# Optimization experiments

Hardware: AMD Instinct MI355X
Metric: run time of the kernel (lower is better)

## Reference

```python
import jax, jax.numpy as jnp
import numpy as np

V, D, H, L, F, S_MAX = 30522, 768, 12, 12, 3072, 512
B, S = 4, 512
HD = D // H
EPS = 1e-5

def setup_inputs():
    key = jax.random.key(0)
    ks = jax.random.split(key, 16)
    s = 0.02
    inp = {
        'input_ids': jax.random.randint(ks[0], (B, S), 0, V),
        'attention_mask': jnp.ones((B, S), dtype=jnp.int32),
        'word_emb': jax.random.normal(ks[1], (V, D)) * s,
        'pos_emb': jax.random.normal(ks[2], (S_MAX, D)) * s,
        'seg_emb': jax.random.normal(ks[3], (2, D)) * s,
        'emb_ln_g': jnp.ones((D,)), 'emb_ln_b': jnp.zeros((D,)),
        # per-layer stacked params, leading dim L
        'Wq': jax.random.normal(ks[4], (L, D, D)) * s,
        'Wk': jax.random.normal(ks[5], (L, D, D)) * s,
        'Wv': jax.random.normal(ks[6], (L, D, D)) * s,
        'Wo': jax.random.normal(ks[7], (L, D, D)) * s,
        'ff1_w': jax.random.normal(ks[8], (L, D, F)) * s,
        'ff1_b': jnp.zeros((L, F)),
        'ff2_w': jax.random.normal(ks[9], (L, F, D)) * s,
        'ff2_b': jnp.zeros((L, D)),
        'ln1_g': jnp.ones((L, D)), 'ln1_b': jnp.zeros((L, D)),
        'ln2_g': jnp.ones((L, D)), 'ln2_b': jnp.zeros((L, D)),
        'out_w': jax.random.normal(ks[10], (D, V)) * s,
        'out_b': jnp.zeros((V,)),
    }
    return inp

def _ln(x, g, b):
    mu = jnp.mean(x, axis=-1, keepdims=True)
    var = jnp.mean(jnp.square(x - mu), axis=-1, keepdims=True)
    return (x - mu) * jax.lax.rsqrt(var + EPS) * g + b

def reference(input_ids, attention_mask, word_emb, pos_emb, seg_emb,
              emb_ln_g, emb_ln_b, Wq, Wk, Wv, Wo, ff1_w, ff1_b, ff2_w, ff2_b,
              ln1_g, ln1_b, ln2_g, ln2_b, out_w, out_b):
    b, s = input_ids.shape
    # embeddings: word + position + segment (segment ids are all zero buffer)
    emb = word_emb[input_ids] + pos_emb[:s][None, :, :] + seg_emb[0][None, None, :]
    x = _ln(emb, emb_ln_g, emb_ln_b)  # [B,S,D]
    # key-position mask: True where masked out. [B,1,1,S]
    neg_mask = (attention_mask == 0)[:, None, None, :]
    scale = 1.0 / jnp.sqrt(jnp.asarray(D, x.dtype))  # NOTE: embed_dim, not head_dim

    def layer(x, p):
        wq, wk, wv, wo, f1w, f1b, f2w, f2b, g1, b1, g2, b2 = p
        q = (x @ wq).reshape(b, s, H, HD)
        k = (x @ wk).reshape(b, s, H, HD)
        v = (x @ wv).reshape(b, s, H, HD)
        scores = jnp.einsum('bqhd,bkhd->bhqk', q, k) * scale  # [B,H,S,S]
        scores = jnp.where(neg_mask, -jnp.inf, scores)
        attn = jax.nn.softmax(scores, axis=-1)
        o = jnp.einsum('bhqk,bkhd->bqhd', attn, v).reshape(b, s, D) @ wo
        x1 = _ln(x + o, g1, b1)
        h = jax.nn.gelu(x1 @ f1w + f1b, approximate=False)  # torch GELU is exact erf
        x2 = _ln(x1 + h @ f2w + f2b, g2, b2)
        return x2, attn

    x, attn_scores = jax.lax.scan(
        layer, x,
        (Wq, Wk, Wv, Wo, ff1_w, ff1_b, ff2_w, ff2_b, ln1_g, ln1_b, ln2_g, ln2_b))
    logits = x @ out_w + out_b  # [B,S,V]
    return logits, attn_scores  # attn_scores: [L,B,H,S,S]
```

## Files before the change

kernel.cpp:

```cpp
#include <hip/hip_runtime.h>
#include <hip/hip_bf16.h>

#define NLAYER 12
#define DMODEL 768
#define NHEAD  12
#define HDIM   64
#define FDIM   3072
#define VOCAB  30522
#define SLEN   512
#define NBATCH 4
#define NTOK   (NBATCH*SLEN)
#define EPSLN  1e-5f

typedef unsigned short u16;
using bf16 = __hip_bfloat16;
typedef __bf16 bf16x8 __attribute__((ext_vector_type(8)));
typedef float  f32x4  __attribute__((ext_vector_type(4)));
typedef u16    u16x4  __attribute__((ext_vector_type(4)));

__device__ __forceinline__ u16 f2bs(float f) {
    bf16 h = __float2bfloat16(f);
    return *reinterpret_cast<u16*>(&h);
}

__device__ __forceinline__ void gload_lds16(const void* g, void* l) {
    auto gp = (const __attribute__((address_space(1))) unsigned int*)g;
    auto lp = (__attribute__((address_space(3))) unsigned int*)(unsigned long long)l;
    __builtin_amdgcn_global_load_lds(gp, lp, 16, 0, 0);
}

template<int N> __device__ __forceinline__ void waitv() {
    if constexpr (N == 0)      asm volatile("s_waitcnt vmcnt(0)" ::: "memory");
    else if constexpr (N == 3) asm volatile("s_waitcnt vmcnt(3)" ::: "memory");
    else if constexpr (N == 4) asm volatile("s_waitcnt vmcnt(4)" ::: "memory");
    else if constexpr (N == 6) asm volatile("s_waitcnt vmcnt(6)" ::: "memory");
    else if constexpr (N == 8) asm volatile("s_waitcnt vmcnt(8)" ::: "memory");
}

__device__ __forceinline__ float wave_sum64(float v) {
#pragma unroll
    for (int off = 32; off > 0; off >>= 1) v += __shfl_down(v, off, 64);
    return v;
}
__device__ __forceinline__ float block_sum256(float v, float* red) {
    v = wave_sum64(v);
    __syncthreads();
    if ((threadIdx.x & 63) == 0) red[threadIdx.x >> 6] = v;
    __syncthreads();
    return red[0] + red[1] + red[2] + red[3];
}

__global__ __launch_bounds__(256) void embed_ln_kernel(
    const int* __restrict__ ids, const float* __restrict__ word,
    const float* __restrict__ pos, const float* __restrict__ seg,
    const float* __restrict__ g, const float* __restrict__ b,
    float* __restrict__ out, u16* __restrict__ outb)
{
    __shared__ float red[4];
    int t = blockIdx.x;
    int s = t & (SLEN - 1);
    long woff = (long)ids[t] * DMODEL;
    float vals[3];
#pragma unroll
    for (int i = 0; i < 3; i++) {
        int d = threadIdx.x + i * 256;
        vals[i] = word[woff + d] + pos[(long)s * DMODEL + d] + seg[d];
    }
    float mu = block_sum256(vals[0] + vals[1] + vals[2], red) * (1.0f / DMODEL);
    float vv = 0.f;
#pragma unroll
    for (int i = 0; i < 3; i++) { float d0 = vals[i] - mu; vv += d0 * d0; }
    float rstd = rsqrtf(block_sum256(vv, red) * (1.0f / DMODEL) + EPSLN);
#pragma unroll
    for (int i = 0; i < 3; i++) {
        int d = threadIdx.x + i * 256;
        float r = (vals[i] - mu) * rstd * g[d] + b[d];
        out[(long)t * DMODEL + d] = r;
        outb[(long)t * DMODEL + d] = f2bs(r);
    }
}

__global__ __launch_bounds__(256) void ln_res2_kernel(
    const float* __restrict__ a, const float* __restrict__ p0,
    const float* __restrict__ p1, const float* __restrict__ cbias,
    const float* __restrict__ g, const float* __restrict__ beta,
    float* __restrict__ out, u16* __restrict__ outb)
{
    __shared__ float red[4];
    long t = blockIdx.x;
    float vals[3];
#pragma unroll
    for (int i = 0; i < 3; i++) {
        int d = threadIdx.x + i * 256;
        float bb = cbias ? cbias[d] : 0.f;
        vals[i] = a[t * DMODEL + d] + p0[t * DMODEL + d] + p1[t * DMODEL + d] + bb;
    }
    float mu = block_sum256(vals[0] + vals[1] + vals[2], red) * (1.0f / DMODEL);
    float vv = 0.f;
#pragma unroll
    for (int i = 0; i < 3; i++) { float d0 = vals[i] - mu; vv += d0 * d0; }
    float rstd = rsqrtf(block_sum256(vv, red) * (1.0f / DMODEL) + EPSLN);
#pragma unroll
    for (int i = 0; i < 3; i++) {
        int d = threadIdx.x + i * 256;
        float r = (vals[i] - mu) * rstd * g[d] + beta[d];
        out[t * DMODEL + d] = r;
        outb[t * DMODEL + d] = f2bs(r);
    }
}

#define DD (DMODEL*DMODEL)
#define DF (DMODEL*FDIM)
#define LAYER_W_ELEMS (4*DD + 2*DF)
#define TILES_DD 576
#define TILES_DF 2304
#define TILES_LAYER (4*TILES_DD + 2*TILES_DF)
#define TILES_ALL (NLAYER*TILES_LAYER)
#define NTX_OW ((VOCAB + 31) / 32)
#define TILES_OW (NTX_OW * (DMODEL/32))

__global__ __launch_bounds__(256) void conv_all_kernel(
    const float* __restrict__ Wq, const float* __restrict__ Wk,
    const float* __restrict__ Wv, const float* __restrict__ Wo,
    const float* __restrict__ F1w, const float* __restrict__ F2w,
    const float* __restrict__ OutW, u16* __restrict__ wT, u16* __restrict__ owT)
{
    __shared__ float t[32][33];
    int id = blockIdx.x;
    const float* src; u16* dst; int K, N, tt;
    if (id < TILES_ALL) {
        int l = id / TILES_LAYER, r = id - l * TILES_LAYER;
        u16* base = wT + (long)l * LAYER_W_ELEMS;
        if (r < TILES_DD)           { src = Wq  + (long)l * DD; dst = base;            K = DMODEL; N = DMODEL; tt = r; }
        else if (r < 2 * TILES_DD)  { src = Wk  + (long)l * DD; dst = base + DD;       K = DMODEL; N = DMODEL; tt = r - TILES_DD; }
        else if (r < 3 * TILES_DD)  { src = Wv  + (long)l * DD; dst = base + 2 * DD;   K = DMODEL; N = DMODEL; tt = r - 2 * TILES_DD; }
        else if (r < 4 * TILES_DD)  { src = Wo  + (long)l * DD; dst = base + 3 * DD;   K = DMODEL; N = DMODEL; tt = r - 3 * TILES_DD; }
        else if (r < 4 * TILES_DD + TILES_DF)
                                    { src = F1w + (long)l * DF; dst = base + 4 * DD;   K = DMODEL; N = FDIM;   tt = r - 4 * TILES_DD; }
        else                        { src = F2w + (long)l * DF; dst = base + 4 * DD + DF; K = FDIM; N = DMODEL; tt = r - 4 * TILES_DD - TILES_DF; }
    } else {
        src = OutW; dst = owT; K = DMODEL; N = VOCAB; tt = id - TILES_ALL;
    }
    int ntx = (N + 31) >> 5;
    int n0 = (tt % ntx) * 32, k0 = (tt / ntx) * 32;
    int tx = threadIdx.x & 31, ty = threadIdx.x >> 5;
#pragma unroll
    for (int i = 0; i < 32; i += 8) {
        int k = k0 + ty + i, n = n0 + tx;
        t[ty + i][tx] = (k < K && n < N) ? src[(long)k * N + n] : 0.f;
    }
    __syncthreads();
#pragma unroll
    for (int i = 0; i < 32; i += 8) {
        int n = n0 + ty + i, k = k0 + tx;
        if (n < N && k < K) dst[(long)n * K + k] = f2bs(t[tx][ty + i]);
    }
}

__global__ __launch_bounds__(256, 2) void attn_kernel(
    const u16* __restrict__ qkvb, const u16* __restrict__ vtb,
    const int* __restrict__ amask,
    float* __restrict__ attn, u16* __restrict__ ob)
{
    __shared__ u16 Qs[64][64];
    __shared__ u16 Ks[SLEN][64];
    __shared__ float maskadd[SLEN];
    __shared__ __align__(16) float redA[64][4];
    __shared__ __align__(16) float redB[64][4];

    u16* Ph = &Ks[0][0];
    u16* Vh = &Ks[256][0];

    int z = blockIdx.y;
    int b = z / NHEAD, h = z - b * NHEAD;
    int m0 = blockIdx.x * 64;
    int tid = threadIdx.x;
    int wave = tid >> 6, lane = tid & 63;
    int quad = lane >> 4, l16 = lane & 15;
    const float scale2 = 0.036084391824351615f * 1.4426950408889634f;

    for (int i = tid; i < SLEN; i += 256)
        maskadd[i] = amask[b * SLEN + i] ? 0.f : -1e30f;

    const u16* Qbase = qkvb + (long)(b * SLEN) * (3 * DMODEL) + h * HDIM;
    const u16* Kbase = Qbase + DMODEL;
    const u16* Vtbase = vtb + (long)z * HDIM * SLEN;

#pragma unroll
    for (int i = 0; i < 2; i++) {
        int off = wave * 2048 + i * 1024 + lane * 16;
        int row = off >> 7, c = (off >> 4) & 7, g = c ^ (row & 7);
        gload_lds16(Qbase + (long)(m0 + row) * (3 * DMODEL) + g * 8,
                    (char*)&Qs[0][0] + wave * 2048 + i * 1024);
    }
#pragma unroll
    for (int i = 0; i < 16; i++) {
        int off = wave * 16384 + i * 1024 + lane * 16;
        int row = off >> 7, c = (off >> 4) & 7, g = c ^ (row & 7);
        gload_lds16(Kbase + (long)row * (3 * DMODEL) + g * 8,
                    (char*)&Ks[0][0] + wave * 16384 + i * 1024);
    }
    __syncthreads();

    f32x4 acc[4][8];
#pragma unroll
    for (int i = 0; i < 4; i++)
#pragma unroll
        for (int j = 0; j < 8; j++) acc[i][j] = (f32x4){0.f, 0.f, 0.f, 0.f};

#pragma unroll
    for (int ks = 0; ks < 2; ks++) {
        bf16x8 afr[4], bfr[8];
#pragma unroll
        for (int i = 0; i < 4; i++) {
            int row = i * 16 + l16;
            int slot = ((ks << 2) + quad) ^ (row & 7);
            afr[i] = *reinterpret_cast<const bf16x8*>((char*)&Qs[0][0] + row * 128 + slot * 16);
        }
#pragma unroll
        for (int j = 0; j < 8; j++) {
            int row = wave * 128 + j * 16 + l16;
            int slot = ((ks << 2) + quad) ^ (row & 7);
            bfr[j] = *reinterpret_cast<const bf16x8*>((char*)&Ks[0][0] + row * 128 + slot * 16);
        }
#pragma unroll
        for (int i = 0; i < 4; i++)
#pragma unroll
            for (int j = 0; j < 8; j++)
                acc[i][j] = __builtin_amdgcn_mfma_f32_16x16x32_bf16(afr[i], bfr[j], acc[i][j], 0, 0, 0);
    }

    {
        float ma[8];
#pragma unroll
        for (int j = 0; j < 8; j++) ma[j] = maskadd[wave * 128 + j * 16 + l16];
#pragma unroll
        for (int i = 0; i < 4; i++)
#pragma unroll
            for (int j = 0; j < 8; j++)
#pragma unroll
                for (int r = 0; r < 4; r++)
                    acc[i][j][r] = acc[i][j][r] * scale2 + ma[j];
    }

    float rmax[4][4];
#pragma unroll
    for (int i = 0; i < 4; i++)
#pragma unroll
        for (int r = 0; r < 4; r++) {
            float m = -3e38f;
#pragma unroll
            for (int j = 0; j < 8; j++) m = fmaxf(m, acc[i][j][r]);
            rmax[i][r] = m;
        }
#pragma unroll
    for (int off = 1; off < 16; off <<= 1)
#pragma unroll
        for (int i = 0; i < 4; i++)
#pragma unroll
            for (int r = 0; r < 4; r++)
                rmax[i][r] = fmaxf(rmax[i][r], __shfl_xor(rmax[i][r], off, 64));
    if (l16 == 0) {
#pragma unroll
        for (int i = 0; i < 4; i++)
#pragma unroll
            for (int r = 0; r < 4; r++) redA[i * 16 + quad * 4 + r][wave] = rmax[i][r];
    }
    __syncthreads();

    {
        const u16* Vb = Vtbase + 0;
#pragma unroll
        for (int i = 0; i < 8; i++) {
            int o = wave * 8192 + i * 1024 + lane * 16;
            int hd = o >> 9, c = (o >> 4) & 31, g = c ^ (hd & 7);
            gload_lds16(Vb + (long)hd * SLEN + g * 8, (char*)Vh + wave * 8192 + i * 1024);
        }
    }

#pragma unroll
    for (int i = 0; i < 4; i++)
#pragma unroll
        for (int r = 0; r < 4; r++) {
            f32x4 v = *reinterpret_cast<const f32x4*>(&redA[i * 16 + quad * 4 + r][0]);
            rmax[i][r] = fmaxf(fmaxf(v[0], v[1]), fmaxf(v[2], v[3]));
        }

    float rsum[4][4];
#pragma unroll
    for (int i = 0; i < 4; i++)
#pragma unroll
        for (int r = 0; r < 4; r++) {
            float s = 0.f;
#pragma unroll
            for (int j = 0; j < 8; j++) {
                float e = __builtin_amdgcn_exp2f(acc[i][j][r] - rmax[i][r]);
                acc[i][j][r] = e;
                s += e;
            }
            rsum[i][r] = s;
        }
#pragma unroll
    for (int off = 1; off < 16; off <<= 1)
#pragma unroll
        for (int i = 0; i < 4; i++)
#pragma unroll
            for (int r = 0; r < 4; r++)
                rsum[i][r] += __shfl_xor(rsum[i][r], off, 64);
    if (l16 == 0) {
#pragma unroll
        for (int i = 0; i < 4; i++)
#pragma unroll
            for (int r = 0; r < 4; r++) redB[i * 16 + quad * 4 + r][wave] = rsum[i][r];
    }
    __syncthreads();

    float* ap = attn + (long)z * SLEN * SLEN;
#pragma unroll
    for (int i = 0; i < 4; i++)
#pragma unroll
        for (int r = 0; r < 4; r++) {
            f32x4 v = *reinterpret_cast<const f32x4*>(&redB[i * 16 + quad * 4 + r][0]);
            float inv = 1.0f / (v[0] + v[1] + v[2] + v[3]);
            long row = m0 + i * 16 + quad * 4 + r;
#pragma unroll
            for (int j = 0; j < 8; j++) {
                int col = (wave << 7) + j * 16 + l16;
                float p = acc[i][j][r] * inv;
                acc[i][j][r] = p;
                ap[row * SLEN + col] = p;
            }
        }

    if (wave < 2) {
#pragma unroll
        for (int i = 0; i < 4; i++)
#pragma unroll
            for (int j = 0; j < 8; j++) {
                int cl = (wave << 7) + j * 16 + l16;
#pragma unroll
                for (int r = 0; r < 4; r++) {
                    int row = i * 16 + quad * 4 + r;
                    int slot = (cl >> 3) ^ (row & 7);
                    *(u16*)((char*)Ph + row * 512 + slot * 16 + (cl & 7) * 2) = f2bs(acc[i][j][r]);
                }
            }
    }
    __syncthreads();

    f32x4 acc2[4];
#pragma unroll
    for (int j = 0; j < 4; j++) acc2[j] = (f32x4){0.f, 0.f, 0.f, 0.f};

#pragma unroll
    for (int step = 0; step < 8; step++) {
        int Prow = (wave << 4) + l16;
        int aslot = (step * 4 + quad) ^ (Prow & 7);
        bf16x8 af = *reinterpret_cast<const bf16x8*>((char*)Ph + Prow * 512 + aslot * 16);
#pragma unroll
        for (int j = 0; j < 4; j++) {
            int hd = j * 16 + l16;
            int bslot = (step * 4 + quad) ^ (hd & 7);
            bf16x8 bf = *reinterpret_cast<const bf16x8*>((char*)Vh + hd * 512 + bslot * 16);
            acc2[j] = __builtin_amdgcn_mfma_f32_16x16x32_bf16(af, bf, acc2[j], 0, 0, 0);
        }
    }
    __syncthreads();

    {
        const u16* Vb = Vtbase + 256;
#pragma unroll
        for (int i = 0; i < 8; i++) {
            int o = wave * 8192 + i * 1024 + lane * 16;
            int hd = o >> 9, c = (o >> 4) & 31, g = c ^ (hd & 7);
            gload_lds16(Vb + (long)hd * SLEN + g * 8, (char*)Vh + wave * 8192 + i * 1024);
        }
    }
    if (wave >= 2) {
#pragma unroll
        for (int i = 0; i < 4; i++)
#pragma unroll
            for (int j = 0; j < 8; j++) {
                int cl = ((wave - 2) << 7) + j * 16 + l16;
#pragma unroll
                for (int r = 0; r < 4; r++) {
                    int row = i * 16 + quad * 4 + r;
                    int slot = (cl >> 3) ^ (row & 7);
                    *(u16*)((char*)Ph + row * 512 + slot * 16 + (cl & 7) * 2) = f2bs(acc[i][j][r]);
                }
            }
    }
    __syncthreads();

#pragma unroll
    for (int step = 0; step < 8; step++) {
        int Prow = (wave << 4) + l16;
        int aslot = (step * 4 + quad) ^ (Prow & 7);
        bf16x8 af = *reinterpret_cast<const bf16x8*>((char*)Ph + Prow * 512 + aslot * 16);
#pragma unroll
        for (int j = 0; j < 4; j++) {
            int hd = j * 16 + l16;
            int bslot = (step * 4 + quad) ^ (hd & 7);
            bf16x8 bf = *reinterpret_cast<const bf16x8*>((char*)Vh + hd * 512 + bslot * 16);
            acc2[j] = __builtin_amdgcn_mfma_f32_16x16x32_bf16(af, bf, acc2[j], 0, 0, 0);
        }
    }

#pragma unroll
    for (int j = 0; j < 4; j++)
#pragma unroll
        for (int r = 0; r < 4; r++) {
            int q = m0 + (wave << 4) + quad * 4 + r;
            ob[((long)(b * SLEN + q)) * DMODEL + h * HDIM + j * 16 + l16] = f2bs(acc2[j][r]);
        }
}

template<int BM, int BN, int OUTBF, int GELU, int QKVF>
__global__ __launch_bounds__(512) void gemm_bf16(
    const u16* __restrict__ A, int lda, long sA1, long sA2,
    const u16* __restrict__ B, int ldb, long sB1, long sB2,
    void* __restrict__ Cv, int ldc, long sC1, long sC2,
    int zdiv, const float* __restrict__ bias,
    int N, int K, float scale, u16* __restrict__ vt)
{
    __shared__ u16 As[2][BM][64];
    __shared__ u16 Bs[2][BN][64];
    int z = blockIdx.z;
    int zq = z / zdiv, zr = z - zq * zdiv;
    A += zq * sA1 + zr * sA2;
    B += zq * sB1 + zr * sB2;

    int nx = gridDim.x, ny = gridDim.y;
    int lin = blockIdx.x + nx * blockIdx.y;
    int nb = nx * ny;
    if ((nb & 7) == 0) lin = (lin & 7) * (nb >> 3) + (lin >> 3);
    int bx = lin % nx, by = lin / nx;

    int m0 = by * BM;
    int n0 = bx * BN;
    int tid = threadIdx.x;
    int wave = tid >> 6, lane = tid & 63;
    int quad = lane >> 4, l16 = lane & 15;
    int wr = wave >> 2, wc = wave & 3;
    constexpr int MR = BM / 32, NR = BN / 64;
    constexpr int PA = BM / 64, PB = BN / 64;
    constexpr int LPT = PA + PB;

    f32x4 acc[MR][NR];
#pragma unroll
    for (int i = 0; i < MR; i++)
#pragma unroll
        for (int j = 0; j < NR; j++) acc[i][j] = (f32x4){0.f, 0.f, 0.f, 0.f};

    auto stage = [&](int buf, int k0) {
#pragma unroll
        for (int p = 0; p < PA; p++) {
            int chunk = p * 512 + tid;
            int row = chunk >> 3, sc = chunk & 7;
            int gcol = (sc ^ (row & 7)) * 8;
            gload_lds16(A + (long)(m0 + row) * lda + k0 + gcol,
                        (char*)&As[buf][0][0] + p * 8192 + wave * 1024);
        }
#pragma unroll
        for (int p = 0; p < PB; p++) {
            int chunk = p * 512 + tid;
            int row = chunk >> 3, sc = chunk & 7;
            int grow = n0 + row;
            if (grow > N - 1) grow = N - 1;
            int gcol = (sc ^ (row & 7)) * 8;
            gload_lds16(B + (long)grow * ldb + k0 + gcol,
                        (char*)&Bs[buf][0][0] + p * 8192 + wave * 1024);
        }
    };

    int nt = K >> 6;
    stage(0, 0);
    if (nt > 1) stage(1, 64);

    for (int t = 0; t < nt; ++t) {
        if (t + 1 < nt) waitv<LPT>();
        else            waitv<0>();
        __builtin_amdgcn_s_barrier();
        __builtin_amdgcn_sched_barrier(0);

        int cur = t & 1;
#pragma unroll
        for (int kh = 0; kh < 2; kh++) {
            bf16x8 afr[MR], bfr[NR];
#pragma unroll
            for (int i = 0; i < MR; i++) {
                int row = wr * (BM / 2) + i * 16 + l16;
                int slot = ((kh << 2) + quad) ^ (row & 7);
                afr[i] = *reinterpret_cast<const bf16x8*>(
                    (char*)&As[cur][0][0] + row * 128 + slot * 16);
            }
#pragma unroll
            for (int j = 0; j < NR; j++) {
                int row = wc * (BN / 4) + j * 16 + l16;
                int slot = ((kh << 2) + quad) ^ (row & 7);
                bfr[j] = *reinterpret_cast<const bf16x8*>(
                    (char*)&Bs[cur][0][0] + row * 128 + slot * 16);
            }
            __builtin_amdgcn_s_setprio(1);
#pragma unroll
            for (int i = 0; i < MR; i++)
#pragma unroll
                for (int j = 0; j < NR; j++)
                    acc[i][j] = __builtin_amdgcn_mfma_f32_16x16x32_bf16(afr[i], bfr[j], acc[i][j], 0, 0, 0);
            __builtin_amdgcn_s_setprio(0);
        }

        asm volatile("" ::: "memory");
        __builtin_amdgcn_sched_barrier(0);
        __builtin_amdgcn_s_barrier();
        __builtin_amdgcn_sched_barrier(0);
        if (t + 2 < nt) stage(cur, (t + 2) << 6);
    }

    float* Cf = (float*)Cv;
    u16*   Cb = (u16*)Cv;
    long coff = zq * sC1 + zr * sC2;
#pragma unroll
    for (int i = 0; i < MR; i++) {
        int rbase = m0 + wr * (BM / 2) + i * 16 + quad * 4;
#pragma unroll
        for (int j = 0; j < NR; j++) {
            int col = n0 + wc * (BN / 4) + j * 16 + l16;
            if (col < N) {
                float badd = bias ? bias[col] : 0.f;
                u16x4 v4;
#pragma unroll
                for (int r = 0; r < 4; r++) {
                    float vv = acc[i][j][r] * scale + badd;
                    if (GELU) vv = 0.5f * vv * (1.0f + erff(vv * 0.70710678118f));
                    long idx = coff + (long)(rbase + r) * ldc + col;
                    if (OUTBF) { u16 u = f2bs(vv); Cb[idx] = u; v4[r] = u; }
                    else       Cf[idx] = vv;
                }
                if (QKVF && col >= 2 * DMODEL) {
                    int hh = (col - 2 * DMODEL) >> 6, hd = col & 63;
                    int bb = rbase >> 9, s = rbase & (SLEN - 1);
                    *reinterpret_cast<u16x4*>(
                        vt + ((long)(bb * NHEAD + hh) * HDIM + hd) * SLEN + s) = v4;
                }
            }
        }
    }
}

template<int BM, int BN, int OUTBF, int GELU, int QKVF = 0>
static inline void launch_gemm(hipStream_t stream,
    const u16* A, int lda, long sA1, long sA2,
    const u16* B, int ldb, long sB1, long sB2,
    void* C, int ldc, long sC1, long sC2,
    int zdiv, const float* bias, int M, int N, int K, float scale, int Z,
    u16* vt = nullptr)
{
    dim3 grid((N + BN - 1) / BN, M / BM, Z);
    gemm_bf16<BM, BN, OUTBF, GELU, QKVF><<<grid, 512, 0, stream>>>(
        A, lda, sA1, sA2, B, ldb, sB1, sB2, C, ldc, sC1, sC2,
        zdiv, bias, N, K, scale, vt);
}

extern "C" void kernel_launch(void* const* d_in, const int* in_sizes, int n_in,
                              void* d_out, int out_size, void* d_ws, size_t ws_size,
                              hipStream_t stream)
{
    const int*   ids   = (const int*)d_in[0];
    const int*   amask = (const int*)d_in[1];
    const float* word  = (const float*)d_in[2];
    const float* pos   = (const float*)d_in[3];
    const float* seg   = (const float*)d_in[4];
    const float* eg    = (const float*)d_in[5];
    const float* eb    = (const float*)d_in[6];
    const float* Wq    = (const float*)d_in[7];
    const float* Wk    = (const float*)d_in[8];
    const float* Wv    = (const float*)d_in[9];
    const float* Wo    = (const float*)d_in[10];
    const float* F1w   = (const float*)d_in[11];
    const float* F1b   = (const float*)d_in[12];
    const float* F2w   = (const float*)d_in[13];
    const float* F2b   = (const float*)d_in[14];
    const float* G1    = (const float*)d_in[15];
    const float* B1    = (const float*)d_in[16];
    const float* G2    = (const float*)d_in[17];
    const float* B2    = (const float*)d_in[18];
    const float* OutW  = (const float*)d_in[19];
    const float* OutB  = (const float*)d_in[20];

    float* logits = (float*)d_out;
    float* attn_base = logits + (long)NTOK * VOCAB;

    long nd = (long)NTOK * DMODEL;
    float* x  = (float*)d_ws;
    float* x1 = x + nd;
    float* p0 = x1 + nd;
    float* p1 = p0 + nd;
    u16* xb   = (u16*)(p1 + nd);
    u16* x1b  = xb + nd;
    u16* qkvb = x1b + nd;
    u16* vtb  = qkvb + (long)NTOK * 3 * DMODEL;
    u16* ob   = vtb + nd;
    u16* hb   = ob + nd;
    u16* wT   = hb + (long)NTOK * FDIM;
    u16* owT  = wT + (long)NLAYER * LAYER_W_ELEMS;

    conv_all_kernel<<<TILES_ALL + TILES_OW, 256, 0, stream>>>(
        Wq, Wk, Wv, Wo, F1w, F2w, OutW, wT, owT);

    embed_ln_kernel<<<NTOK, 256, 0, stream>>>(ids, word, pos, seg, eg, eb, x, xb);

    for (int l = 0; l < NLAYER; l++) {
        const u16* qkvT = wT + (long)l * LAYER_W_ELEMS;
        const u16* woT  = qkvT + 3 * DD;
        const u16* f1T  = qkvT + 4 * DD;
        const u16* f2T  = qkvT + 4 * DD + DF;
        const float* f1b = F1b + (long)l * FDIM;
        const float* f2b = F2b + (long)l * DMODEL;
        float* attn_l = attn_base + (long)l * NBATCH * NHEAD * SLEN * SLEN;

        launch_gemm<128, 64, 1, 0, 1>(stream, xb, DMODEL, 0, 0,
                                      qkvT, DMODEL, 0, 0,
                                      qkvb, 3 * DMODEL, 0, 0,
                                      1, nullptr, NTOK, 3 * DMODEL, DMODEL, 1.f, 1, vtb);

        attn_kernel<<<dim3(SLEN / 64, NBATCH * NHEAD), 256, 0, stream>>>(
            qkvb, vtb, amask, attn_l, ob);

        launch_gemm<128, 64, 0, 0>(stream, ob, DMODEL, 384, 0,
                                   woT, DMODEL, 384, 0,
                                   p0, DMODEL, nd, 0,
                                   1, nullptr, NTOK, DMODEL, 384, 1.f, 2);

        ln_res2_kernel<<<NTOK, 256, 0, stream>>>(x, p0, p1, nullptr,
                                                 G1 + (long)l * DMODEL, B1 + (long)l * DMODEL, x1, x1b);

        launch_gemm<128, 64, 1, 1>(stream, x1b, DMODEL, 0, 0,
                                   f1T, DMODEL, 0, 0,
                                   hb, FDIM, 0, 0,
                                   1, f1b, NTOK, FDIM, DMODEL, 1.f, 1);

        launch_gemm<128, 64, 0, 0>(stream, hb, FDIM, 1536, 0,
                                   f2T, FDIM, 1536, 0,
                                   p0, DMODEL, nd, 0,
                                   1, nullptr, NTOK, DMODEL, 1536, 1.f, 2);

        ln_res2_kernel<<<NTOK, 256, 0, stream>>>(x1, p0, p1, f2b,
                                                 G2 + (long)l * DMODEL, B2 + (long)l * DMODEL, x, xb);
    }

    launch_gemm<128, 128, 0, 0>(stream, xb, DMODEL, 0, 0,
                                owT, DMODEL, 0, 0,
                                logits, VOCAB, 0, 0,
                                1, OutB, NTOK, VOCAB, DMODEL, 1.f, 1);
}
```

Measured before the change: 1.755 ms.

## Use persistent pipelined GEMM for vocab projection and drop tile swizzle

Replaces the final logits GEMM with a persistent kernel of 512 blocks. Each block walks a strided list of 128x128 tiles, and the double-buffered LDS pipeline keeps prefetching across tile boundaries so the prologue and epilogue are not exposed once per tile. Separately, the generic GEMM no longer remaps block indices in groups of 8 and uses plain blockIdx ordering, which changes L2 locality for every layer GEMM. The persistent kernel writes fp32 outputs inside the k loop, and plain ordering may reduce cache reuse in the other GEMMs.

```diff
diff --git a/kernel.cpp b/kernel.cpp
--- a/kernel.cpp
+++ b/kernel.cpp
@@ -430,14 +430,8 @@
     A += zq * sA1 + zr * sA2;
     B += zq * sB1 + zr * sB2;
 
-    int nx = gridDim.x, ny = gridDim.y;
-    int lin = blockIdx.x + nx * blockIdx.y;
-    int nb = nx * ny;
-    if ((nb & 7) == 0) lin = (lin & 7) * (nb >> 3) + (lin >> 3);
-    int bx = lin % nx, by = lin / nx;
-
-    int m0 = by * BM;
-    int n0 = bx * BN;
+    int m0 = blockIdx.y * BM;
+    int n0 = blockIdx.x * BN;
     int tid = threadIdx.x;
     int wave = tid >> 6, lane = tid & 63;
     int quad = lane >> 4, l16 = lane & 15;
@@ -560,6 +554,131 @@
     gemm_bf16<BM, BN, OUTBF, GELU, QKVF><<<grid, 512, 0, stream>>>(
         A, lda, sA1, sA2, B, ldb, sB1, sB2, C, ldc, sC1, sC2,
         zdiv, bias, N, K, scale, vt);
+}
+
+template<int BM, int BN>
+__global__ __launch_bounds__(512) void gemm_pers(
+    const u16* __restrict__ A, int lda,
+    const u16* __restrict__ B, int ldb,
+    float* __restrict__ C, int ldc,
+    const float* __restrict__ bias,
+    int N, int K, int ntiles, int nx)
+{
+    __shared__ u16 As[2][BM][64];
+    __shared__ u16 Bs[2][BN][64];
+    int tid = threadIdx.x;
+    int wave = tid >> 6, lane = tid & 63;
+    int quad = lane >> 4, l16 = lane & 15;
+    int wr = wave >> 2, wc = wave & 3;
+    constexpr int MR = BM / 32, NR = BN / 64;
+    constexpr int PA = BM / 64, PB = BN / 64;
+    constexpr int LPT = PA + PB;
+
+    int G = gridDim.x;
+    int nt = K >> 6;
+    if ((int)blockIdx.x >= ntiles) return;
+    int myTiles = (ntiles - 1 - (int)blockIdx.x) / G + 1;
+    int steps = myTiles * nt;
+
+    f32x4 acc[MR][NR];
+#pragma unroll
+    for (int i = 0; i < MR; i++)
+#pragma unroll
+        for (int j = 0; j < NR; j++) acc[i][j] = (f32x4){0.f, 0.f, 0.f, 0.f};
+
+    int sg = blockIdx.x, sk = 0;
+    auto stageC = [&](int buf) {
+        int by = sg / nx, bx = sg - by * nx;
+        int m0 = by * BM, n0 = bx * BN;
+        int k0 = sk << 6;
+#pragma unroll
+        for (int p = 0; p < PA; p++) {
+            int chunk = p * 512 + tid;
+            int row = chunk >> 3, sc = chunk & 7;
+            int gcol = (sc ^ (row & 7)) * 8;
+            gload_lds16(A + (long)(m0 + row) * lda + k0 + gcol,
+                        (char*)&As[buf][0][0] + p * 8192 + wave * 1024);
+        }
+#pragma unroll
+        for (int p = 0; p < PB; p++) {
+            int chunk = p * 512 + tid;
+            int row = chunk >> 3, sc = chunk & 7;
+            int grow = n0 + row;
+            if (grow > N - 1) grow = N - 1;
+            int gcol = (sc ^ (row & 7)) * 8;
+            gload_lds16(B + (long)grow * ldb + k0 + gcol,
+                        (char*)&Bs[buf][0][0] + p * 8192 + wave * 1024);
+        }
+        if (++sk == nt) { sk = 0; sg += G; }
+    };
+
+    stageC(0);
+    if (steps > 1) stageC(1);
+
+    int cg = blockIdx.x, ck = 0;
+    for (int s = 0; s < steps; ++s) {
+        if (s + 1 < steps) waitv<LPT>();
+        else               waitv<0>();
+        __builtin_amdgcn_s_barrier();
+        __builtin_amdgcn_sched_barrier(0);
+
+        int cur = s & 1;
+#pragma unroll
+        for (int kh = 0; kh < 2; kh++) {
+            bf16x8 afr[MR], bfr[NR];
+#pragma unroll
+            for (int i = 0; i < MR; i++) {
+                int row = wr * (BM / 2) + i * 16 + l16;
+                int slot = ((kh << 2) + quad) ^ (row & 7);
+                afr[i] = *reinterpret_cast<const bf16x8*>(
+                    (char*)&As[cur][0][0] + row * 128 + slot * 16);
+            }
+#pragma unroll
+            for (int j = 0; j < NR; j++) {
+                int row = wc * (BN / 4) + j * 16 + l16;
+                int slot = ((kh << 2) + quad) ^ (row & 7);
+                bfr[j] = *reinterpret_cast<const bf16x8*>(
+                    (char*)&Bs[cur][0][0] + row * 128 + slot * 16);
+            }
+            __builtin_amdgcn_s_setprio(1);
+#pragma unroll
+            for (int i = 0; i < MR; i++)
+#pragma unroll
+                for (int j = 0; j < NR; j++)
+                    acc[i][j] = __builtin_amdgcn_mfma_f32_16x16x32_bf16(afr[i], bfr[j], acc[i][j], 0, 0, 0);
+            __builtin_amdgcn_s_setprio(0);
+        }
+
+        asm volatile("" ::: "memory");
+        __builtin_amdgcn_sched_barrier(0);
+        __builtin_amdgcn_s_barrier();
+        __builtin_amdgcn_sched_barrier(0);
+        if (s + 2 < steps) stageC(cur);
+
+        if (ck == nt - 1) {
+            int by = cg / nx, bx = cg - by * nx;
+            int m0 = by * BM, n0 = bx * BN;
+#pragma unroll
+            for (int i = 0; i < MR; i++) {
+                int rbase = m0 + wr * (BM / 2) + i * 16 + quad * 4;
+#pragma unroll
+                for (int j = 0; j < NR; j++) {
+                    int col = n0 + wc * (BN / 4) + j * 16 + l16;
+                    if (col < N) {
+                        float badd = bias[col];
+#pragma unroll
+                        for (int r = 0; r < 4; r++)
+                            C[(long)(rbase + r) * ldc + col] = acc[i][j][r] + badd;
+                    }
+#pragma unroll
+                    for (int r = 0; r < 4; r++) acc[i][j][r] = 0.f;
+                }
+            }
+            ck = 0; cg += G;
+        } else {
+            ++ck;
+        }
+    }
 }
 
 extern "C" void kernel_launch(void* const* d_in, const int* in_sizes, int n_in,
@@ -649,8 +768,10 @@
                                                  G2 + (long)l * DMODEL, B2 + (long)l * DMODEL, x, xb);
     }
 
-    launch_gemm<128, 128, 0, 0>(stream, xb, DMODEL, 0, 0,
-                                owT, DMODEL, 0, 0,
-                                logits, VOCAB, 0, 0,
-                                1, OutB, NTOK, VOCAB, DMODEL, 1.f, 1);
-}
+    {
+        int nx = (VOCAB + 127) / 128;
+        int ntiles = nx * (NTOK / 128);
+        gemm_pers<128, 128><<<512, 512, 0, stream>>>(
+            xb, DMODEL, owT, DMODEL, logits, VOCAB, OutB, VOCAB, DMODEL, ntiles, nx);
+    }
+}
```

After: 1.693 ms (median of 2 runs). -3.5%, faster.
